# Performance work log

Hardware: AMD Instinct MI355X
Metric: run time of the kernel (lower is better)

## Reference

```python
import jax, jax.numpy as jnp
import numpy as np

N, NFEAT, NHID, NCLASS, NLAYERS = 8192, 512, 128, 40, 3
NEG = -9e15

def _sparse_adj(key, n, density=0.002):
    u = jax.random.uniform(key, (n, n), dtype=jnp.float32)
    return jnp.where(u < density, u / density, 0.0)

def setup_inputs() -> dict:
    key = jax.random.key(0)
    ks = jax.random.split(key, 12)
    return {
        "x": jax.random.normal(ks[0], (N, NFEAT), dtype=jnp.float32),
        "adj1": _sparse_adj(ks[1], N),
        "adj2": _sparse_adj(ks[2], N),
        "adj_att": _sparse_adj(ks[3], N),
        "fc1_w": jax.random.normal(ks[4], (NLAYERS, NHID, NFEAT), dtype=jnp.float32) * (1.0 / np.sqrt(NFEAT)),
        "fc1_b": jnp.zeros((NLAYERS, NHID), jnp.float32),
        "Q_w": jax.random.normal(ks[5], (NLAYERS - 1, NHID, NHID), dtype=jnp.float32) * (1.0 / np.sqrt(NHID)),
        "Q_b": jnp.zeros((NLAYERS - 1, NHID), jnp.float32),
        "K_w": jax.random.normal(ks[6], (NLAYERS - 1, NHID, NHID), dtype=jnp.float32) * (1.0 / np.sqrt(NHID)),
        "K_b": jnp.zeros((NLAYERS - 1, NHID), jnp.float32),
        "hop_select": jnp.ones((NLAYERS,), jnp.float32),
        "w": jnp.ones((NLAYERS - 1, 2), jnp.float32),
        "clf_w": jax.random.normal(ks[7], (NCLASS, NHID * NLAYERS), dtype=jnp.float32) * (1.0 / np.sqrt(NHID * NLAYERS)),
        "clf_b": jnp.zeros((NCLASS,), jnp.float32),
    }

def _l2_normalize(x, eps=1e-12):
    # F.normalize(x, p=2, dim=1)
    n = jnp.sqrt(jnp.sum(x * x, axis=1, keepdims=True))
    return x / jnp.maximum(n, eps)

def reference(x, adj1, adj2, adj_att, fc1_w, fc1_b, Q_w, Q_b, K_w, K_b,
              hop_select, w, clf_w, clf_b):
    adj_list = [None, adj1, adj2]
    mask = jax.nn.softmax(hop_select)  # hop selection weights, shape [nlayers]
    outs = []
    for i in range(NLAYERS):
        tmp = x @ fc1_w[i].T + fc1_b[i]  # [N, nhid]
        if adj_list[i] is not None:
            adj = adj_list[i]
            W_att = jax.nn.softmax(w[i - 1])  # [2]
            tmp_att = adj_att @ tmp           # [N, nhid]
            # GCN1: linear then propagate with adj_att (act='None')
            Q = adj_att @ (tmp_att @ Q_w[i - 1].T + Q_b[i - 1])
            K = adj_att @ (tmp_att @ K_w[i - 1].T + K_b[i - 1])
            scores = Q @ K.T                  # [N, N]
            scores = jnp.where(adj > 0, scores, NEG)
            attention = jax.nn.softmax(scores, axis=-1) * W_att[0] + adj * W_att[1]
            tmp = attention @ tmp             # [N, nhid]
        tmp = _l2_normalize(tmp)
        outs.append(mask[i] * tmp)
    final = jnp.concatenate(outs, axis=1)     # [N, nhid*nlayers]
    out = jax.nn.relu(final) @ clf_w.T + clf_b  # dropout is identity in eval
    return jax.nn.log_softmax(out, axis=1)
```

## Files before the change

kernel.cpp:

```cpp
#include <hip/hip_runtime.h>
#include <hip/hip_bf16.h>

#define NN     8192
#define NF4    2048
#define NFEAT  512
#define NHID   128
#define NCLASS 40
#define NLAY   3
#define CAPA   128
#define FSZ    ((size_t)NN * NHID)

typedef float f32x4 __attribute__((ext_vector_type(4)));

__global__ __launch_bounds__(256, 4) void k_scanA_fc1(
    const float* __restrict__ x, const float* __restrict__ fc1w, const float* __restrict__ fc1b,
    const float* __restrict__ adjA, const float* __restrict__ hop, const float* __restrict__ w,
    float* __restrict__ tmps, float* __restrict__ f_mask, float* __restrict__ f_watt,
    float* __restrict__ colsum, float* __restrict__ rowsumA,
    int* __restrict__ cnts, int* __restrict__ colsArr, float* __restrict__ valsArr)
{
    __shared__ float smem[3200];
    const int bx = blockIdx.x, tid = threadIdx.x;

    if (bx < 384) {
        float* As = smem;
        float* Bs = smem + 1088;
        const int tx = tid & 15, ty = tid >> 4;
        const int bm = (bx & 127) * 64;
        const int layer = bx >> 7;
        const int bn = layer * 128;
        float acc[4][8] = {};

        const int rA = tid >> 2, cA = (tid & 3) * 4;
        for (int kt = 0; kt < NFEAT; kt += 16) {
            f32x4 va = *reinterpret_cast<const f32x4*>(&x[(size_t)(bm + rA) * NFEAT + kt + cA]);
            As[(cA + 0) * 68 + rA] = va[0];
            As[(cA + 1) * 68 + rA] = va[1];
            As[(cA + 2) * 68 + rA] = va[2];
            As[(cA + 3) * 68 + rA] = va[3];
            #pragma unroll
            for (int it = 0; it < 2; ++it) {
                int L = tid + it * 256;
                int r = L >> 2, c4 = (L & 3) * 4;
                f32x4 vb = *reinterpret_cast<const f32x4*>(&fc1w[(size_t)(bn + r) * NFEAT + kt + c4]);
                Bs[(c4 + 0) * 132 + r] = vb[0];
                Bs[(c4 + 1) * 132 + r] = vb[1];
                Bs[(c4 + 2) * 132 + r] = vb[2];
                Bs[(c4 + 3) * 132 + r] = vb[3];
            }
            __syncthreads();
            #pragma unroll
            for (int kk = 0; kk < 16; ++kk) {
                f32x4 ra  = *reinterpret_cast<const f32x4*>(&As[kk * 68 + ty * 4]);
                f32x4 rb0 = *reinterpret_cast<const f32x4*>(&Bs[kk * 132 + tx * 4]);
                f32x4 rb1 = *reinterpret_cast<const f32x4*>(&Bs[kk * 132 + tx * 4 + 64]);
                #pragma unroll
                for (int i = 0; i < 4; ++i) {
                    #pragma unroll
                    for (int j = 0; j < 4; ++j) {
                        acc[i][j]     = fmaf(ra[i], rb0[j], acc[i][j]);
                        acc[i][j + 4] = fmaf(ra[i], rb1[j], acc[i][j + 4]);
                    }
                }
            }
            __syncthreads();
        }
        const float* bofs = fc1b + bn;
        #pragma unroll
        for (int i = 0; i < 4; ++i) {
            int m = bm + ty * 4 + i;
            #pragma unroll
            for (int j = 0; j < 8; ++j) {
                int lc = (j < 4) ? (tx * 4 + j) : (64 + tx * 4 + (j - 4));
                tmps[(size_t)layer * FSZ + (size_t)m * NHID + lc] = acc[i][j] + bofs[lc];
            }
        }
    } else if (bx < 384 + NN) {
        const int row = bx - 384;
        int* s_lcnt = (int*)smem;
        float* s_lsum = smem + 1;
        if (tid == 0) { *s_lcnt = 0; *s_lsum = 0.f; }
        __syncthreads();
        const f32x4* arow = reinterpret_cast<const f32x4*>(adjA + (size_t)row * NN);
        int* rc = colsArr + (size_t)row * CAPA;
        float* rv = valsArr + (size_t)row * CAPA;

        f32x4 v[8];
        #pragma unroll
        for (int i = 0; i < 8; ++i) v[i] = arow[tid + (i << 8)];

        float ls = 0.f;
        #pragma unroll
        for (int i = 0; i < 8; ++i) {
            const int c4 = tid + (i << 8);
            #pragma unroll
            for (int k = 0; k < 4; ++k) {
                if (v[i][k] > 0.f) {
                    int p = atomicAdd(s_lcnt, 1);
                    if (p < CAPA) { rc[p] = c4 * 4 + k; rv[p] = v[i][k]; }
                    ls += v[i][k];
                }
            }
        }
        if (ls != 0.f) atomicAdd(s_lsum, ls);
        __syncthreads();
        if (tid == 0) {
            int n = *s_lcnt;
            cnts[row] = n < CAPA ? n : CAPA;
            rowsumA[row] = *s_lsum;
        }
    } else {
        colsum[tid] = 0.f;
        if (tid == 0) {
            float m = fmaxf(fmaxf(hop[0], hop[1]), hop[2]);
            float e0 = expf(hop[0] - m), e1 = expf(hop[1] - m), e2 = expf(hop[2] - m);
            float s = e0 + e1 + e2;
            f_mask[0] = e0 / s; f_mask[1] = e1 / s; f_mask[2] = e2 / s;
            for (int l = 0; l < 2; ++l) {
                float a = w[2 * l], b = w[2 * l + 1];
                float mm = fmaxf(a, b);
                float ea = expf(a - mm), eb = expf(b - mm);
                float ss = ea + eb;
                f_watt[2 * l] = ea / ss; f_watt[2 * l + 1] = eb / ss;
            }
        }
    }
}

__global__ __launch_bounds__(128) void k_spmm_cs(
    const int* __restrict__ cnts, const int* __restrict__ colsArr, const float* __restrict__ valsArr,
    const float* __restrict__ tmps, float* __restrict__ tmp_att, float* __restrict__ colsum)
{
    int bx = blockIdx.x, L = blockIdx.y, t = threadIdx.x;
    if (bx >= NN) {
        int c = bx - NN;
        const float* X = tmps + (size_t)(L + 1) * FSZ + (size_t)c * 128 * NHID;
        float a = 0.f;
        for (int r = 0; r < 128; ++r) a += X[(size_t)r * NHID + t];
        atomicAdd(&colsum[L * NHID + t], a);
        return;
    }
    int row = bx;
    const float* X = tmps + (size_t)(L + 1) * FSZ;
    float* Y = tmp_att + (size_t)L * FSZ;
    __shared__ int sc[CAPA];
    __shared__ float sv[CAPA];
    int n = cnts[row];
    for (int p = t; p < n; p += 128) { sc[p] = colsArr[(size_t)row * CAPA + p]; sv[p] = valsArr[(size_t)row * CAPA + p]; }
    __syncthreads();
    float a0 = 0.f, a1 = 0.f, a2 = 0.f, a3 = 0.f;
    int p = 0;
    for (; p + 4 <= n; p += 4) {
        a0 = fmaf(sv[p],     X[(size_t)sc[p]     * NHID + t], a0);
        a1 = fmaf(sv[p + 1], X[(size_t)sc[p + 1] * NHID + t], a1);
        a2 = fmaf(sv[p + 2], X[(size_t)sc[p + 2] * NHID + t], a2);
        a3 = fmaf(sv[p + 3], X[(size_t)sc[p + 3] * NHID + t], a3);
    }
    for (; p < n; ++p) a0 = fmaf(sv[p], X[(size_t)sc[p] * NHID + t], a0);
    Y[(size_t)row * NHID + t] = (a0 + a1) + (a2 + a3);
}

__global__ __launch_bounds__(256, 4) void k_scan12_t2(
    const int* __restrict__ cnts, const int* __restrict__ colsArr, const float* __restrict__ valsArr,
    const float* __restrict__ tmp_att, const float* __restrict__ Qw, const float* __restrict__ Kw,
    const float* __restrict__ Qb, const float* __restrict__ Kb,
    const float* __restrict__ rowsumA, float* __restrict__ QKm,
    const float* __restrict__ adj1, const float* __restrict__ adj2,
    int* __restrict__ cntsOut, int* __restrict__ colsOut, float* __restrict__ valsOut)
{
    __shared__ float AsT[8192];
    const int b = blockIdx.x, tid = threadIdx.x;

    if (b < 256) {
        const int bm = (b & 127) * 64, Lz = b >> 7;
        const float* X = tmp_att + (size_t)Lz * FSZ;
        {
            const int lrow = tid >> 2, coff = (tid & 3) * 32;
            const int row = bm + lrow;
            f32x4 acc[8] = {};
            const int n = cnts[row];
            const int* rc = colsArr + (size_t)row * CAPA;
            const float* rv = valsArr + (size_t)row * CAPA;
            for (int p = 0; p < n; ++p) {
                int c = rc[p];
                float v = rv[p];
                const f32x4* src = reinterpret_cast<const f32x4*>(X + (size_t)c * NHID + coff);
                #pragma unroll
                for (int j = 0; j < 8; ++j) {
                    f32x4 s = src[j];
                    acc[j][0] = fmaf(v, s[0], acc[j][0]);
                    acc[j][1] = fmaf(v, s[1], acc[j][1]);
                    acc[j][2] = fmaf(v, s[2], acc[j][2]);
                    acc[j][3] = fmaf(v, s[3], acc[j][3]);
                }
            }
            #pragma unroll
            for (int j = 0; j < 8; ++j)
                #pragma unroll
                for (int q = 0; q < 4; ++q)
                    AsT[(coff + j * 4 + q) * 64 + lrow] = acc[j][q];
        }
        __syncthreads();

        const int tx = tid & 15, ty = tid >> 4;
        float rs[4];
        #pragma unroll
        for (int i = 0; i < 4; ++i) rs[i] = rowsumA[bm + ty * 4 + i];
        float* C = QKm + (size_t)Lz * NN * 256;

        #pragma unroll
        for (int ch = 0; ch < 4; ++ch) {
            const int bn = ch * 64;
            const float* Bp; const float* bp; int bc;
            if (bn < 128) { Bp = Qw + (size_t)Lz * NHID * NHID; bp = Qb + (size_t)Lz * NHID; bc = bn; }
            else          { Bp = Kw + (size_t)Lz * NHID * NHID; bp = Kb + (size_t)Lz * NHID; bc = bn - 128; }
            float acc[4][4] = {};
            for (int k4 = 0; k4 < NHID; k4 += 4) {
                f32x4 wv[4];
                #pragma unroll
                for (int j = 0; j < 4; ++j)
                    wv[j] = *reinterpret_cast<const f32x4*>(&Bp[(size_t)(bc + tx * 4 + j) * NHID + k4]);
                #pragma unroll
                for (int q = 0; q < 4; ++q) {
                    f32x4 ra = *reinterpret_cast<const f32x4*>(&AsT[(k4 + q) * 64 + ty * 4]);
                    #pragma unroll
                    for (int i = 0; i < 4; ++i)
                        #pragma unroll
                        for (int j = 0; j < 4; ++j)
                            acc[i][j] = fmaf(ra[i], wv[j][q], acc[i][j]);
                }
            }
            #pragma unroll
            for (int i = 0; i < 4; ++i) {
                int m = bm + ty * 4 + i;
                #pragma unroll
                for (int j = 0; j < 4; ++j) {
                    int nc = bn + tx * 4 + j;
                    C[(size_t)m * 256 + nc] = acc[i][j] + rs[i] * bp[bc + tx * 4 + j];
                }
            }
        }
    } else {
        const int e = b - 256;
        const int mat = e >> 13, row = e & (NN - 1);
        const float* adj = mat ? adj2 : adj1;
        int* s_lcnt = (int*)AsT;
        if (tid == 0) *s_lcnt = 0;
        __syncthreads();
        const f32x4* arow = reinterpret_cast<const f32x4*>(adj + (size_t)row * NN);
        int* rc = colsOut + (size_t)(mat * NN + row) * CAPA;
        float* rv = valsOut + (size_t)(mat * NN + row) * CAPA;

        f32x4 v[8];
        #pragma unroll
        for (int i = 0; i < 8; ++i) v[i] = arow[tid + (i << 8)];

        #pragma unroll
        for (int i = 0; i < 8; ++i) {
            const int c4 = tid + (i << 8);
            #pragma unroll
            for (int k = 0; k < 4; ++k) {
                if (v[i][k] > 0.f) {
                    int p = atomicAdd(s_lcnt, 1);
                    if (p < CAPA) { rc[p] = c4 * 4 + k; rv[p] = v[i][k]; }
                }
            }
        }
        __syncthreads();
        if (tid == 0) {
            int n = *s_lcnt;
            cntsOut[mat * NN + row] = n < CAPA ? n : CAPA;
        }
    }
}

__global__ __launch_bounds__(256) void k_attn_clf(
    const int* __restrict__ cnts12, const int* __restrict__ cols12, const float* __restrict__ vals12,
    const float* __restrict__ QKm, const float* __restrict__ tmps,
    const float* __restrict__ colsum, const float* __restrict__ watt,
    const float* __restrict__ mask, const float* __restrict__ Wc, const float* __restrict__ bc,
    float* __restrict__ out)
{
    const int row = blockIdx.x, t = threadIdx.x;
    const int h = t >> 7, ht = t & 127;
    __shared__ int cols[2][CAPA];
    __shared__ float avals[2][CAPA];
    __shared__ float svals[2][CAPA];
    __shared__ __align__(16) float qrow[2][NHID];
    __shared__ float ws[4];
    __shared__ float ws0[2];
    __shared__ float fin[NHID * NLAY];
    __shared__ float cpart[2][64];

    const float* QK = QKm + (size_t)h * NN * 256;
    const float* T = tmps + (size_t)(h + 1) * FSZ;
    const int n = cnts12[h * NN + row];
    const int* rc = cols12 + (size_t)(h * NN + row) * CAPA;
    const float* rv = vals12 + (size_t)(h * NN + row) * CAPA;

    for (int p = ht; p < n; p += 128) { cols[h][p] = rc[p]; avals[h][p] = rv[p]; }
    if (ht < 32) *reinterpret_cast<f32x4*>(&qrow[h][ht * 4]) =
        *reinterpret_cast<const f32x4*>(QK + (size_t)row * 256 + ht * 4);
    __syncthreads();

    const float W0 = watt[h * 2], W1 = watt[h * 2 + 1];

    if (n > 0) {
        int g = ht >> 5, sl = ht & 31;
        f32x4 qv = *reinterpret_cast<const f32x4*>(&qrow[h][sl * 4]);
        for (int p = g; p < n; p += 4) {
            f32x4 kv = *reinterpret_cast<const f32x4*>(QK + (size_t)cols[h][p] * 256 + 128 + sl * 4);
            float s = qv[0] * kv[0] + qv[1] * kv[1] + qv[2] * kv[2] + qv[3] * kv[3];
            #pragma unroll
            for (int m = 16; m; m >>= 1) s += __shfl_xor(s, m);
            if (sl == 0) svals[h][p] = s;
        }
    }
    __syncthreads();

    if (n > 0 && ht < 64) {
        float mx = -3.0e38f;
        for (int p = ht; p < n; p += 64) mx = fmaxf(mx, svals[h][p]);
        #pragma unroll
        for (int m = 32; m; m >>= 1) mx = fmaxf(mx, __shfl_xor(mx, m));
        float ss = 0.f;
        for (int p = ht; p < n; p += 64) ss += expf(svals[h][p] - mx);
        #pragma unroll
        for (int m = 32; m; m >>= 1) ss += __shfl_xor(ss, m);
        float inv = 1.0f / ss;
        for (int p = ht; p < n; p += 64) avals[h][p] = expf(svals[h][p] - mx) * inv * W0 + avals[h][p] * W1;
    }
    __syncthreads();

    float acc = 0.f;
    if (n > 0) {
        float a1 = 0.f;
        int p = 0;
        for (; p + 2 <= n; p += 2) {
            acc = fmaf(avals[h][p],     T[(size_t)cols[h][p]     * NHID + ht], acc);
            a1  = fmaf(avals[h][p + 1], T[(size_t)cols[h][p + 1] * NHID + ht], a1);
        }
        if (p < n) acc = fmaf(avals[h][p], T[(size_t)cols[h][p] * NHID + ht], acc);
        acc += a1;
    } else {
        acc = W0 * (1.0f / (float)NN) * colsum[h * NHID + ht];
    }

    float s2 = acc * acc;
    #pragma unroll
    for (int m = 32; m; m >>= 1) s2 += __shfl_xor(s2, m);
    if ((t & 63) == 0) ws[t >> 6] = s2;

    float v0 = 0.f;
    if (t < 128) {
        v0 = tmps[(size_t)row * NHID + t];
        float s0 = v0 * v0;
        #pragma unroll
        for (int m = 32; m; m >>= 1) s0 += __shfl_xor(s0, m);
        if ((t & 63) == 0) ws0[t >> 6] = s0;
    }
    __syncthreads();

    {
        float d = fmaxf(sqrtf(ws[h * 2] + ws[h * 2 + 1]), 1e-12f);
        fin[(h + 1) * NHID + ht] = fmaxf(mask[h + 1] * acc / d, 0.f);
        if (t < 128) {
            float d0 = fmaxf(sqrtf(ws0[0] + ws0[1]), 1e-12f);
            fin[t] = fmaxf(mask[0] * v0 / d0, 0.f);
        }
    }
    __syncthreads();

    const int wv = t >> 6, lane = t & 63;
    if (wv < 2 && lane < NCLASS) {
        const float* wrow = Wc + (size_t)lane * (NHID * NLAY) + wv * 192;
        const float* fi = fin + wv * 192;
        float a0 = 0.f, a1 = 0.f, a2 = 0.f, a3 = 0.f;
        #pragma unroll 4
        for (int k = 0; k < 192; k += 4) {
            a0 = fmaf(fi[k],     wrow[k],     a0);
            a1 = fmaf(fi[k + 1], wrow[k + 1], a1);
            a2 = fmaf(fi[k + 2], wrow[k + 2], a2);
            a3 = fmaf(fi[k + 3], wrow[k + 3], a3);
        }
        cpart[wv][lane] = (a0 + a1) + (a2 + a3);
    }
    __syncthreads();

    if (t < 64) {
        float logit = (t < NCLASS) ? (cpart[0][t] + cpart[1][t] + bc[t]) : -3.0e38f;
        float mx = logit;
        #pragma unroll
        for (int m = 32; m; m >>= 1) mx = fmaxf(mx, __shfl_xor(mx, m));
        float e = (t < NCLASS) ? expf(logit - mx) : 0.f;
        float ssum = e;
        #pragma unroll
        for (int m = 32; m; m >>= 1) ssum += __shfl_xor(ssum, m);
        if (t < NCLASS) out[(size_t)row * NCLASS + t] = logit - mx - logf(ssum);
    }
}

extern "C" void kernel_launch(void* const* d_in, const int* in_sizes, int n_in,
                              void* d_out, int out_size, void* d_ws, size_t ws_size,
                              hipStream_t stream) {
    const float* x       = (const float*)d_in[0];
    const float* adj1    = (const float*)d_in[1];
    const float* adj2    = (const float*)d_in[2];
    const float* adj_att = (const float*)d_in[3];
    const float* fc1_w   = (const float*)d_in[4];
    const float* fc1_b   = (const float*)d_in[5];
    const float* Q_w     = (const float*)d_in[6];
    const float* Q_b     = (const float*)d_in[7];
    const float* K_w     = (const float*)d_in[8];
    const float* K_b     = (const float*)d_in[9];
    const float* hop     = (const float*)d_in[10];
    const float* w       = (const float*)d_in[11];
    const float* clf_w   = (const float*)d_in[12];
    const float* clf_b   = (const float*)d_in[13];

    float* W = (float*)d_ws;
    float* f_mask   = W;
    float* f_watt   = W + 4;
    float* f_colsum = W + 8;
    float* rowsumA  = W + 264;
    float* tmps     = W + 264 + NN;
    float* tmp_att  = tmps + 3 * FSZ;
    float* QKm      = tmp_att + 2 * FSZ;
    float* csr_valsA = QKm + 4 * FSZ;
    float* csr_vals12 = csr_valsA + FSZ;
    int*   csr_colsA = (int*)(csr_vals12 + 2 * FSZ);
    int*   csr_cols12 = csr_colsA + FSZ;
    int*   csr_cntA  = csr_cols12 + 2 * FSZ;
    int*   csr_cnt12 = csr_cntA + NN;

    size_t need = (size_t)((char*)(csr_cnt12 + 2 * NN) - (char*)d_ws);
    if (ws_size < need) return;

    k_scanA_fc1<<<384 + NN + 1, 256, 0, stream>>>(
        x, fc1_w, fc1_b, adj_att, hop, w,
        tmps, f_mask, f_watt, f_colsum, rowsumA, csr_cntA, csr_colsA, csr_valsA);

    k_spmm_cs<<<dim3(NN + 64, 2), 128, 0, stream>>>(
        csr_cntA, csr_colsA, csr_valsA, tmps, tmp_att, f_colsum);

    k_scan12_t2<<<256 + 2 * NN, 256, 0, stream>>>(
        csr_cntA, csr_colsA, csr_valsA, tmp_att, Q_w, K_w, Q_b, K_b, rowsumA, QKm,
        adj1, adj2, csr_cnt12, csr_cols12, csr_vals12);

    k_attn_clf<<<NN, 256, 0, stream>>>(
        csr_cnt12, csr_cols12, csr_vals12, QKm, tmps, f_colsum, f_watt, f_mask,
        clf_w, clf_b, (float*)d_out);
}
```

Baseline: 339.7 us.

## Scan multiple adjacency rows per block with register double-buffered prefetch

```diff
diff --git a/kernel.cpp b/kernel.cpp
--- a/kernel.cpp
+++ b/kernel.cpp
@@ -9,6 +9,7 @@
 #define NLAY   3
 #define CAPA   128
 #define FSZ    ((size_t)NN * NHID)
+#define ROWS_PER_BLK 8
 
 typedef float f32x4 __attribute__((ext_vector_type(4)));
 
@@ -75,39 +76,49 @@
                 tmps[(size_t)layer * FSZ + (size_t)m * NHID + lc] = acc[i][j] + bofs[lc];
             }
         }
-    } else if (bx < 384 + NN) {
-        const int row = bx - 384;
+    } else if (bx < 384 + NN / ROWS_PER_BLK) {
+        const int row0 = (bx - 384) * ROWS_PER_BLK;
         int* s_lcnt = (int*)smem;
         float* s_lsum = smem + 1;
-        if (tid == 0) { *s_lcnt = 0; *s_lsum = 0.f; }
-        __syncthreads();
-        const f32x4* arow = reinterpret_cast<const f32x4*>(adjA + (size_t)row * NN);
-        int* rc = colsArr + (size_t)row * CAPA;
-        float* rv = valsArr + (size_t)row * CAPA;
-
-        f32x4 v[8];
-        #pragma unroll
-        for (int i = 0; i < 8; ++i) v[i] = arow[tid + (i << 8)];
-
-        float ls = 0.f;
-        #pragma unroll
-        for (int i = 0; i < 8; ++i) {
-            const int c4 = tid + (i << 8);
-            #pragma unroll
-            for (int k = 0; k < 4; ++k) {
-                if (v[i][k] > 0.f) {
-                    int p = atomicAdd(s_lcnt, 1);
-                    if (p < CAPA) { rc[p] = c4 * 4 + k; rv[p] = v[i][k]; }
-                    ls += v[i][k];
-                }
-            }
-        }
-        if (ls != 0.f) atomicAdd(s_lsum, ls);
-        __syncthreads();
-        if (tid == 0) {
-            int n = *s_lcnt;
-            cnts[row] = n < CAPA ? n : CAPA;
-            rowsumA[row] = *s_lsum;
+        f32x4 A[8], B[8];
+        {
+            const f32x4* arow = reinterpret_cast<const f32x4*>(adjA + (size_t)row0 * NN);
+            #pragma unroll
+            for (int j = 0; j < 8; ++j) A[j] = arow[tid + (j << 8)];
+        }
+        for (int i = 0; i < ROWS_PER_BLK; ++i) {
+            const int row = row0 + i;
+            if (i + 1 < ROWS_PER_BLK) {
+                const f32x4* nrow = reinterpret_cast<const f32x4*>(adjA + (size_t)(row + 1) * NN);
+                #pragma unroll
+                for (int j = 0; j < 8; ++j) B[j] = nrow[tid + (j << 8)];
+            }
+            if (tid == 0) { *s_lcnt = 0; *s_lsum = 0.f; }
+            __syncthreads();
+            int* rc = colsArr + (size_t)row * CAPA;
+            float* rv = valsArr + (size_t)row * CAPA;
+            float ls = 0.f;
+            #pragma unroll
+            for (int j = 0; j < 8; ++j) {
+                const int c4 = tid + (j << 8);
+                #pragma unroll
+                for (int k = 0; k < 4; ++k) {
+                    if (A[j][k] > 0.f) {
+                        int p = atomicAdd(s_lcnt, 1);
+                        if (p < CAPA) { rc[p] = c4 * 4 + k; rv[p] = A[j][k]; }
+                        ls += A[j][k];
+                    }
+                }
+            }
+            if (ls != 0.f) atomicAdd(s_lsum, ls);
+            __syncthreads();
+            if (tid == 0) {
+                int n = *s_lcnt;
+                cnts[row] = n < CAPA ? n : CAPA;
+                rowsumA[row] = *s_lsum;
+            }
+            #pragma unroll
+            for (int j = 0; j < 8; ++j) A[j] = B[j];
         }
     } else {
         colsum[tid] = 0.f;
@@ -241,35 +252,46 @@
             }
         }
     } else {
-        const int e = b - 256;
-        const int mat = e >> 13, row = e & (NN - 1);
+        const int e0 = (b - 256) * ROWS_PER_BLK;
+        const int mat = e0 >> 13;
+        const int row0 = e0 & (NN - 1);
         const float* adj = mat ? adj2 : adj1;
         int* s_lcnt = (int*)AsT;
-        if (tid == 0) *s_lcnt = 0;
-        __syncthreads();
-        const f32x4* arow = reinterpret_cast<const f32x4*>(adj + (size_t)row * NN);
-        int* rc = colsOut + (size_t)(mat * NN + row) * CAPA;
-        float* rv = valsOut + (size_t)(mat * NN + row) * CAPA;
-
-        f32x4 v[8];
-        #pragma unroll
-        for (int i = 0; i < 8; ++i) v[i] = arow[tid + (i << 8)];
-
-        #pragma unroll
-        for (int i = 0; i < 8; ++i) {
-            const int c4 = tid + (i << 8);
-            #pragma unroll
-            for (int k = 0; k < 4; ++k) {
-                if (v[i][k] > 0.f) {
-                    int p = atomicAdd(s_lcnt, 1);
-                    if (p < CAPA) { rc[p] = c4 * 4 + k; rv[p] = v[i][k]; }
-                }
-            }
-        }
-        __syncthreads();
-        if (tid == 0) {
-            int n = *s_lcnt;
-            cntsOut[mat * NN + row] = n < CAPA ? n : CAPA;
+        f32x4 A[8], B[8];
+        {
+            const f32x4* arow = reinterpret_cast<const f32x4*>(adj + (size_t)row0 * NN);
+            #pragma unroll
+            for (int j = 0; j < 8; ++j) A[j] = arow[tid + (j << 8)];
+        }
+        for (int i = 0; i < ROWS_PER_BLK; ++i) {
+            const int row = row0 + i;
+            if (i + 1 < ROWS_PER_BLK) {
+                const f32x4* nrow = reinterpret_cast<const f32x4*>(adj + (size_t)(row + 1) * NN);
+                #pragma unroll
+                for (int j = 0; j < 8; ++j) B[j] = nrow[tid + (j << 8)];
+            }
+            if (tid == 0) *s_lcnt = 0;
+            __syncthreads();
+            int* rc = colsOut + (size_t)(mat * NN + row) * CAPA;
+            float* rv = valsOut + (size_t)(mat * NN + row) * CAPA;
+            #pragma unroll
+            for (int j = 0; j < 8; ++j) {
+                const int c4 = tid + (j << 8);
+                #pragma unroll
+                for (int k = 0; k < 4; ++k) {
+                    if (A[j][k] > 0.f) {
+                        int p = atomicAdd(s_lcnt, 1);
+                        if (p < CAPA) { rc[p] = c4 * 4 + k; rv[p] = A[j][k]; }
+                    }
+                }
+            }
+            __syncthreads();
+            if (tid == 0) {
+                int n = *s_lcnt;
+                cntsOut[mat * NN + row] = n < CAPA ? n : CAPA;
+            }
+            #pragma unroll
+            for (int j = 0; j < 8; ++j) A[j] = B[j];
         }
     }
 }
@@ -436,14 +458,14 @@
     size_t need = (size_t)((char*)(csr_cnt12 + 2 * NN) - (char*)d_ws);
     if (ws_size < need) return;
 
-    k_scanA_fc1<<<384 + NN + 1, 256, 0, stream>>>(
+    k_scanA_fc1<<<384 + NN / ROWS_PER_BLK + 1, 256, 0, stream>>>(
         x, fc1_w, fc1_b, adj_att, hop, w,
         tmps, f_mask, f_watt, f_colsum, rowsumA, csr_cntA, csr_colsA, csr_valsA);
 
     k_spmm_cs<<<dim3(NN + 64, 2), 128, 0, stream>>>(
         csr_cntA, csr_colsA, csr_valsA, tmps, tmp_att, f_colsum);
 
-    k_scan12_t2<<<256 + 2 * NN, 256, 0, stream>>>(
+    k_scan12_t2<<<256 + 2 * NN / ROWS_PER_BLK, 256, 0, stream>>>(
         csr_cntA, csr_colsA, csr_valsA, tmp_att, Q_w, K_w, Q_b, K_b, rowsumA, QKm,
         adj1, adj2, csr_cnt12, csr_cols12, csr_vals12);
 
```

New measurement: 373.1 us. 1.1x slower.

## Rebalance adjacency scans across kernels and merge spmm heads into one block

Applied to the files above, without the earlier changes.

```diff
diff --git a/kernel.cpp b/kernel.cpp
--- a/kernel.cpp
+++ b/kernel.cpp
@@ -2,7 +2,6 @@
 #include <hip/hip_bf16.h>
 
 #define NN     8192
-#define NF4    2048
 #define NFEAT  512
 #define NHID   128
 #define NCLASS 40
@@ -12,12 +11,12 @@
 
 typedef float f32x4 __attribute__((ext_vector_type(4)));
 
-__global__ __launch_bounds__(256, 4) void k_scanA_fc1(
+__global__ __launch_bounds__(256, 8) void k_d1(
     const float* __restrict__ x, const float* __restrict__ fc1w, const float* __restrict__ fc1b,
     const float* __restrict__ adjA, const float* __restrict__ hop, const float* __restrict__ w,
     float* __restrict__ tmps, float* __restrict__ f_mask, float* __restrict__ f_watt,
     float* __restrict__ colsum, float* __restrict__ rowsumA,
-    int* __restrict__ cnts, int* __restrict__ colsArr, float* __restrict__ valsArr)
+    int* __restrict__ cntsA, int* __restrict__ colsA, float* __restrict__ valsA)
 {
     __shared__ float smem[3200];
     const int bx = blockIdx.x, tid = threadIdx.x;
@@ -82,8 +81,8 @@
         if (tid == 0) { *s_lcnt = 0; *s_lsum = 0.f; }
         __syncthreads();
         const f32x4* arow = reinterpret_cast<const f32x4*>(adjA + (size_t)row * NN);
-        int* rc = colsArr + (size_t)row * CAPA;
-        float* rv = valsArr + (size_t)row * CAPA;
+        int* rc = colsA + (size_t)row * CAPA;
+        float* rv = valsA + (size_t)row * CAPA;
 
         f32x4 v[8];
         #pragma unroll
@@ -106,7 +105,7 @@
         __syncthreads();
         if (tid == 0) {
             int n = *s_lcnt;
-            cnts[row] = n < CAPA ? n : CAPA;
+            cntsA[row] = n < CAPA ? n : CAPA;
             rowsumA[row] = *s_lsum;
         }
     } else {
@@ -127,46 +126,76 @@
     }
 }
 
-__global__ __launch_bounds__(128) void k_spmm_cs(
-    const int* __restrict__ cnts, const int* __restrict__ colsArr, const float* __restrict__ valsArr,
-    const float* __restrict__ tmps, float* __restrict__ tmp_att, float* __restrict__ colsum)
+__global__ __launch_bounds__(256, 8) void k_d2(
+    const int* __restrict__ cntsA, const int* __restrict__ colsA, const float* __restrict__ valsA,
+    const float* __restrict__ tmps, float* __restrict__ tmp_att, float* __restrict__ colsum,
+    const float* __restrict__ adj1,
+    int* __restrict__ cnts12, int* __restrict__ cols12, float* __restrict__ vals12)
 {
-    int bx = blockIdx.x, L = blockIdx.y, t = threadIdx.x;
-    if (bx >= NN) {
-        int c = bx - NN;
-        const float* X = tmps + (size_t)(L + 1) * FSZ + (size_t)c * 128 * NHID;
-        float a = 0.f;
-        for (int r = 0; r < 128; ++r) a += X[(size_t)r * NHID + t];
-        atomicAdd(&colsum[L * NHID + t], a);
-        return;
-    }
-    int row = bx;
-    const float* X = tmps + (size_t)(L + 1) * FSZ;
-    float* Y = tmp_att + (size_t)L * FSZ;
     __shared__ int sc[CAPA];
     __shared__ float sv[CAPA];
-    int n = cnts[row];
-    for (int p = t; p < n; p += 128) { sc[p] = colsArr[(size_t)row * CAPA + p]; sv[p] = valsArr[(size_t)row * CAPA + p]; }
-    __syncthreads();
-    float a0 = 0.f, a1 = 0.f, a2 = 0.f, a3 = 0.f;
-    int p = 0;
-    for (; p + 4 <= n; p += 4) {
-        a0 = fmaf(sv[p],     X[(size_t)sc[p]     * NHID + t], a0);
-        a1 = fmaf(sv[p + 1], X[(size_t)sc[p + 1] * NHID + t], a1);
-        a2 = fmaf(sv[p + 2], X[(size_t)sc[p + 2] * NHID + t], a2);
-        a3 = fmaf(sv[p + 3], X[(size_t)sc[p + 3] * NHID + t], a3);
-    }
-    for (; p < n; ++p) a0 = fmaf(sv[p], X[(size_t)sc[p] * NHID + t], a0);
-    Y[(size_t)row * NHID + t] = (a0 + a1) + (a2 + a3);
+    __shared__ int s_lcnt;
+    const int bx = blockIdx.x, t = threadIdx.x;
+
+    if (bx < NN) {
+        const int row = bx;
+        const int n = cntsA[row];
+        for (int p = t; p < n; p += 256) { sc[p] = colsA[(size_t)row * CAPA + p]; sv[p] = valsA[(size_t)row * CAPA + p]; }
+        __syncthreads();
+        const int h = t >> 7, col = t & 127;
+        const float* X = tmps + (size_t)(h + 1) * FSZ;
+        float a0 = 0.f, a1 = 0.f, a2 = 0.f, a3 = 0.f;
+        int p = 0;
+        for (; p + 4 <= n; p += 4) {
+            a0 = fmaf(sv[p],     X[(size_t)sc[p]     * NHID + col], a0);
+            a1 = fmaf(sv[p + 1], X[(size_t)sc[p + 1] * NHID + col], a1);
+            a2 = fmaf(sv[p + 2], X[(size_t)sc[p + 2] * NHID + col], a2);
+            a3 = fmaf(sv[p + 3], X[(size_t)sc[p + 3] * NHID + col], a3);
+        }
+        for (; p < n; ++p) a0 = fmaf(sv[p], X[(size_t)sc[p] * NHID + col], a0);
+        tmp_att[(size_t)h * FSZ + (size_t)row * NHID + col] = (a0 + a1) + (a2 + a3);
+    } else if (bx < NN + 64) {
+        const int c = bx - NN;
+        const int h = t >> 7, col = t & 127;
+        const float* X = tmps + (size_t)(h + 1) * FSZ + (size_t)c * 128 * NHID;
+        float a = 0.f;
+        for (int r = 0; r < 128; ++r) a += X[(size_t)r * NHID + col];
+        atomicAdd(&colsum[h * NHID + col], a);
+    } else {
+        const int row = bx - NN - 64;
+        if (t == 0) s_lcnt = 0;
+        __syncthreads();
+        const f32x4* arow = reinterpret_cast<const f32x4*>(adj1 + (size_t)row * NN);
+        int* rc = cols12 + (size_t)row * CAPA;
+        float* rv = vals12 + (size_t)row * CAPA;
+
+        f32x4 v[8];
+        #pragma unroll
+        for (int i = 0; i < 8; ++i) v[i] = arow[t + (i << 8)];
+
+        #pragma unroll
+        for (int i = 0; i < 8; ++i) {
+            const int c4 = t + (i << 8);
+            #pragma unroll
+            for (int k = 0; k < 4; ++k) {
+                if (v[i][k] > 0.f) {
+                    int p = atomicAdd(&s_lcnt, 1);
+                    if (p < CAPA) { rc[p] = c4 * 4 + k; rv[p] = v[i][k]; }
+                }
+            }
+        }
+        __syncthreads();
+        if (t == 0) cnts12[row] = s_lcnt < CAPA ? s_lcnt : CAPA;
+    }
 }
 
-__global__ __launch_bounds__(256, 4) void k_scan12_t2(
-    const int* __restrict__ cnts, const int* __restrict__ colsArr, const float* __restrict__ valsArr,
+__global__ __launch_bounds__(256, 4) void k_d3(
+    const int* __restrict__ cntsA, const int* __restrict__ colsA, const float* __restrict__ valsA,
     const float* __restrict__ tmp_att, const float* __restrict__ Qw, const float* __restrict__ Kw,
     const float* __restrict__ Qb, const float* __restrict__ Kb,
     const float* __restrict__ rowsumA, float* __restrict__ QKm,
-    const float* __restrict__ adj1, const float* __restrict__ adj2,
-    int* __restrict__ cntsOut, int* __restrict__ colsOut, float* __restrict__ valsOut)
+    const float* __restrict__ adj2,
+    int* __restrict__ cnts12, int* __restrict__ cols12, float* __restrict__ vals12)
 {
     __shared__ float AsT[8192];
     const int b = blockIdx.x, tid = threadIdx.x;
@@ -178,9 +207,9 @@
             const int lrow = tid >> 2, coff = (tid & 3) * 32;
             const int row = bm + lrow;
             f32x4 acc[8] = {};
-            const int n = cnts[row];
-            const int* rc = colsArr + (size_t)row * CAPA;
-            const float* rv = valsArr + (size_t)row * CAPA;
+            const int n = cntsA[row];
+            const int* rc = colsA + (size_t)row * CAPA;
+            const float* rv = valsA + (size_t)row * CAPA;
             for (int p = 0; p < n; ++p) {
                 int c = rc[p];
                 float v = rv[p];
@@ -241,15 +270,13 @@
             }
         }
     } else {
-        const int e = b - 256;
-        const int mat = e >> 13, row = e & (NN - 1);
-        const float* adj = mat ? adj2 : adj1;
+        const int row = b - 256;
         int* s_lcnt = (int*)AsT;
         if (tid == 0) *s_lcnt = 0;
         __syncthreads();
-        const f32x4* arow = reinterpret_cast<const f32x4*>(adj + (size_t)row * NN);
-        int* rc = colsOut + (size_t)(mat * NN + row) * CAPA;
-        float* rv = valsOut + (size_t)(mat * NN + row) * CAPA;
+        const f32x4* arow = reinterpret_cast<const f32x4*>(adj2 + (size_t)row * NN);
+        int* rc = cols12 + (size_t)(NN + row) * CAPA;
+        float* rv = vals12 + (size_t)(NN + row) * CAPA;
 
         f32x4 v[8];
         #pragma unroll
@@ -267,10 +294,7 @@
             }
         }
         __syncthreads();
-        if (tid == 0) {
-            int n = *s_lcnt;
-            cntsOut[mat * NN + row] = n < CAPA ? n : CAPA;
-        }
+        if (tid == 0) cnts12[NN + row] = *s_lcnt < CAPA ? *s_lcnt : CAPA;
     }
 }
 
@@ -436,16 +460,17 @@
     size_t need = (size_t)((char*)(csr_cnt12 + 2 * NN) - (char*)d_ws);
     if (ws_size < need) return;
 
-    k_scanA_fc1<<<384 + NN + 1, 256, 0, stream>>>(
+    k_d1<<<384 + NN + 1, 256, 0, stream>>>(
         x, fc1_w, fc1_b, adj_att, hop, w,
         tmps, f_mask, f_watt, f_colsum, rowsumA, csr_cntA, csr_colsA, csr_valsA);
 
-    k_spmm_cs<<<dim3(NN + 64, 2), 128, 0, stream>>>(
-        csr_cntA, csr_colsA, csr_valsA, tmps, tmp_att, f_colsum);
-
-    k_scan12_t2<<<256 + 2 * NN, 256, 0, stream>>>(
+    k_d2<<<NN + 64 + NN, 256, 0, stream>>>(
+        csr_cntA, csr_colsA, csr_valsA, tmps, tmp_att, f_colsum,
+        adj1, csr_cnt12, csr_cols12, csr_vals12);
+
+    k_d3<<<256 + NN, 256, 0, stream>>>(
         csr_cntA, csr_colsA, csr_valsA, tmp_att, Q_w, K_w, Q_b, K_b, rowsumA, QKm,
-        adj1, adj2, csr_cnt12, csr_cols12, csr_vals12);
+        adj2, csr_cnt12, csr_cols12, csr_vals12);
 
     k_attn_clf<<<NN, 256, 0, stream>>>(
         csr_cnt12, csr_cols12, csr_vals12, QKm, tmps, f_colsum, f_watt, f_mask,
```

After: 416.4 us. +22.6%, slower.
